# Kernel tuning notes

Measured on AMD Instinct MI355X. Metric: run time of the kernel, lower is better.

Reference implementation:

```python
import math
import jax, jax.numpy as jnp
import numpy as np

L = 4        # number of base-MLP layers
B = 16       # batch of weight-space samples
N = 256      # base-MLP width (n_in = n_out = N)
C_IN = 16    # input channels per weight entry
C_OUT = 16   # output channels per weight entry
HID = 64     # siren hidden dim
W0 = 1.0
W0_FIRST = 30.0
FINAL_NORM = math.sqrt((2 * L + 7) * C_IN)


def setup_inputs() -> dict:
    key = jax.random.key(0)
    ks = jax.random.split(key, 17)
    d = {}
    for i in range(L):
        d[f"w{i}"] = jax.random.normal(ks[i], (B, N, N, C_IN), jnp.float32) * 0.02
        d[f"b{i}"] = jax.random.normal(ks[L + i], (B, N, C_IN), jnp.float32) * 0.02
    def u(k, shape, scale):
        return jax.random.uniform(k, shape, jnp.float32, -scale, scale)
    # SIREN-style init scales
    d["s_w0"] = u(ks[8], (3, HID), 1.0 / 3.0)
    d["s_b0"] = u(ks[9], (HID,), 1.0 / math.sqrt(3.0))
    d["s_w1"] = u(ks[10], (HID, HID), math.sqrt(6.0 / HID) / W0)
    d["s_b1"] = u(ks[11], (HID,), 1.0 / math.sqrt(HID))
    d["s_w2"] = u(ks[12], (HID, HID), math.sqrt(6.0 / HID) / W0)
    d["s_b2"] = u(ks[13], (HID,), 1.0 / math.sqrt(HID))
    d["s_wo"] = u(ks[14], (HID, C_IN * C_OUT), math.sqrt(6.0 / HID) / W0)
    d["s_bo"] = u(ks[15], (C_IN * C_OUT,), 1.0 / math.sqrt(HID))
    return d


def _siren(x, sp):
    sw0, sb0, sw1, sb1, sw2, sb2, swo, sbo = sp
    h = jnp.sin(W0_FIRST * (x @ sw0 + sb0))
    h = jnp.sin(W0 * (h @ sw1 + sb1))
    h = jnp.sin(W0 * (h @ sw2 + sb2))
    return (h @ swo + sbo) / FINAL_NORM


def _forward(ws, bs, sp):
    term_idx = jnp.linspace(-1.0, 1.0, num=14)
    layer_idx = jnp.linspace(-1.0, 1.0, num=L)
    grid = jnp.stack(jnp.meshgrid(layer_idx, layer_idx, indexing='ij'), axis=-1)  # (L,L,2)

    g_in = jnp.concatenate([jnp.broadcast_to(grid, (4, L, L, 2)),
                            jnp.broadcast_to(term_idx[:4, None, None, None], (4, L, L, 1))], -1)
    global_terms = _siren(g_in, sp).reshape(4, L, L, C_IN, C_OUT)

    dgrid = jnp.transpose(jnp.diagonal(grid))          # (L,2)
    d_in = jnp.concatenate([jnp.broadcast_to(dgrid, (6, L, 2)),
                            jnp.broadcast_to(term_idx[4:10, None, None], (6, L, 1))], -1)
    diag_terms = _siren(d_in, sp).reshape(6, L, C_IN, C_OUT)

    p1 = jnp.transpose(jnp.diagonal(grid, offset=1))   # (L-1,2)
    p1_in = jnp.concatenate([jnp.broadcast_to(p1, (2, L - 1, 2)),
                             jnp.broadcast_to(term_idx[10:12, None, None], (2, L - 1, 1))], -1)
    diag_p1 = _siren(p1_in, sp).reshape(2, L - 1, C_IN, C_OUT)

    m1 = jnp.transpose(jnp.diagonal(grid, offset=-1))  # (L-1,2)
    m1_in = jnp.concatenate([jnp.broadcast_to(m1, (2, L - 1, 2)),
                             jnp.broadcast_to(term_idx[12:14, None, None], (2, L - 1, 1))], -1)
    diag_m1 = _siren(m1_in, sp).reshape(2, L - 1, C_IN, C_OUT)

    t_w_otherw, t_w_otherb = global_terms[0], global_terms[1]
    t_b_otherw, t_b_otherb = global_terms[2], global_terms[3]
    t_w_wrow, t_w_wcol, t_w_w = diag_terms[0], diag_terms[1], diag_terms[2]
    t_w_b, t_b_wcol, t_bb = diag_terms[3], diag_terms[4], diag_terms[5]
    t_w_wm1, t_w_bm1 = diag_m1[0], diag_m1[1]
    t_w_wp1, t_b_wp1 = diag_p1[0], diag_p1[1]

    rsums = [jnp.mean(w, axis=1) for w in ws]          # (B,K,c)
    csums = [jnp.mean(w, axis=2) for w in ws]          # (B,J,c)
    allsums = jnp.stack([jnp.mean(r, axis=1) for r in rsums], -1)  # (B,c,L)
    sums_b = jnp.stack([jnp.mean(b, axis=1) for b in bs], -1)      # (B,c,L)

    outs = []
    for i in range(L):
        ow = jnp.einsum('bjkc,cd->bjkd', ws[i], t_w_w[i])
        ow += jnp.einsum('bcl,lcd->bd', allsums, t_w_otherw[i])[:, None, None, :]
        ow += jnp.einsum('bcl,lcd->bd', sums_b, t_w_otherb[i])[:, None, None, :]
        ow += jnp.einsum('bjc,cd->bjd', csums[i], t_w_wcol[i])[:, :, None, :]
        ow += jnp.einsum('bkc,cd->bkd', rsums[i], t_w_wrow[i])[:, None, :, :]
        ow += jnp.einsum('bkc,cd->bkd', bs[i], t_w_b[i])[:, None, :, :]
        if i > 0:
            ow += jnp.einsum('bjc,cd->bjd', rsums[i - 1], t_w_wm1[i - 1])[:, :, None, :]
            ow += jnp.einsum('bjc,cd->bjd', bs[i - 1], t_w_bm1[i - 1])[:, :, None, :]
        if i < L - 1:
            ow += jnp.einsum('bkc,cd->bkd', csums[i + 1], t_w_wp1[i])[:, None, :, :]
        ob = jnp.einsum('bjc,cd->bjd', bs[i], t_bb[i])
        ob += jnp.einsum('bkc,cd->bkd', rsums[i], t_b_wcol[i])
        if i < L - 1:
            ob += jnp.einsum('bkc,cd->bkd', csums[i + 1], t_b_wp1[i])
        ob += jnp.einsum('bcl,lcd->bd', allsums, t_b_otherw[i])[:, None, :]
        ob += jnp.einsum('bcl,lcd->bd', sums_b, t_b_otherb[i])[:, None, :]
        outs += [ow, ob]
    return tuple(outs)


def reference(w0, w1, w2, w3, b0, b1, b2, b3,
              s_w0, s_b0, s_w1, s_b1, s_w2, s_b2, s_wo, s_bo):
    return _forward([w0, w1, w2, w3], [b0, b1, b2, b3],
                    (s_w0, s_b0, s_w1, s_b1, s_w2, s_b2, s_wo, s_bo))
```

## Files before the change

### kernel.cpp

```cpp
#include <hip/hip_runtime.h>
#include <math.h>

#define DEV_INLINE __device__ __forceinline__

constexpr int Nn = 256;
constexpr size_t SZW = (size_t)16 * 256 * 256 * 16;
constexpr size_t SZB = (size_t)16 * 256 * 16;
constexpr size_t OSTRIDE = SZW + SZB;

constexpr int T_GT = 0;
constexpr int T_DT = 16384;
constexpr int T_P1 = 22528;
constexpr int T_M1 = 24064;
constexpr int O_RS = 25600;
constexpr int O_CS = 287744;
constexpr int O_AS = 549888;
constexpr int O_BS = 550912;
constexpr int O_AROW = 551936;
constexpr int O_BCOL = 814080;

DEV_INLINE void f4acc(float4& a, const float4 b) { a.x += b.x; a.y += b.y; a.z += b.z; a.w += b.w; }
DEV_INLINE float4 f4add(const float4 a, const float4 b) { return make_float4(a.x + b.x, a.y + b.y, a.z + b.z, a.w + b.w); }
DEV_INLINE void f4fma(float4& a, float s, const float4 t) {
    a.x = fmaf(s, t.x, a.x); a.y = fmaf(s, t.y, a.y);
    a.z = fmaf(s, t.z, a.z); a.w = fmaf(s, t.w, a.w);
}

__global__ __launch_bounds__(64) void siren_kernel(
    const float* __restrict__ sw0, const float* __restrict__ sb0,
    const float* __restrict__ sw1, const float* __restrict__ sb1,
    const float* __restrict__ sw2, const float* __restrict__ sb2,
    const float* __restrict__ swo, const float* __restrict__ sbo,
    float* __restrict__ ws) {
    __shared__ float h[64];
    const int p = blockIdx.x, t = threadIdx.x;
    const float lv[4] = {-1.f, -1.f / 3.f, 1.f / 3.f, 1.f};
    float x, y, tt;
    if (p < 64)      { int tm = p >> 4, a = (p >> 2) & 3, bb = p & 3; x = lv[a];   y = lv[bb];  tt = -1.f + 2.f * tm / 13.f; }
    else if (p < 88) { int q = p - 64; int tm = q >> 2, a = q & 3;    x = lv[a];   y = lv[a];   tt = -1.f + 2.f * (4 + tm) / 13.f; }
    else if (p < 94) { int q = p - 88; int tm = q / 3, a = q % 3;     x = lv[a];   y = lv[a+1]; tt = -1.f + 2.f * (10 + tm) / 13.f; }
    else             { int q = p - 94; int tm = q / 3, a = q % 3;     x = lv[a+1]; y = lv[a];   tt = -1.f + 2.f * (12 + tm) / 13.f; }
    float v = sinf(30.f * (x * sw0[t] + y * sw0[64 + t] + tt * sw0[128 + t] + sb0[t]));
    h[t] = v; __syncthreads();
    float v1 = sb1[t];
    for (int u = 0; u < 64; ++u) v1 += h[u] * sw1[u * 64 + t];
    v1 = sinf(v1);
    __syncthreads(); h[t] = v1; __syncthreads();
    float v2 = sb2[t];
    for (int u = 0; u < 64; ++u) v2 += h[u] * sw2[u * 64 + t];
    v2 = sinf(v2);
    __syncthreads(); h[t] = v2; __syncthreads();
    const float inv_fn = 0.06454972243679028f;
    for (int m = 0; m < 4; ++m) {
        int o = m * 64 + t;
        float vo = sbo[o];
        for (int u = 0; u < 64; ++u) vo += h[u] * swo[u * 256 + o];
        ws[p * 256 + o] = vo * inv_fn;
    }
}

__global__ __launch_bounds__(64) void reduce_b_kernel(
    const float4* __restrict__ b0, const float4* __restrict__ b1,
    const float4* __restrict__ b2, const float4* __restrict__ b3,
    float* __restrict__ ws) {
    const int z = blockIdx.x;
    const int l = z >> 4, b = z & 15;
    const float4* bp = ((l == 0) ? b0 : (l == 1) ? b1 : (l == 2) ? b2 : b3) + (size_t)b * Nn * 4;
    const int lane = threadIdx.x;
    const int c4 = lane & 3, part = lane >> 2;
    float4 acc = make_float4(0.f, 0.f, 0.f, 0.f);
    for (int s = 0; s < 16; ++s) f4acc(acc, bp[(size_t)(part + s * 16) * 4 + c4]);
#pragma unroll
    for (int m = 4; m < 64; m <<= 1) {
        acc.x += __shfl_xor(acc.x, m); acc.y += __shfl_xor(acc.y, m);
        acc.z += __shfl_xor(acc.z, m); acc.w += __shfl_xor(acc.w, m);
    }
    if (lane < 4) {
        float* dst = ws + O_BS + (size_t)z * 16 + lane * 4;
        dst[0] = acc.x; dst[1] = acc.y; dst[2] = acc.z; dst[3] = acc.w;
    }
}

__global__ __launch_bounds__(256) void reduce_w_kernel(
    const float4* __restrict__ w0, const float4* __restrict__ w1,
    const float4* __restrict__ w2, const float4* __restrict__ w3,
    float* __restrict__ ws, int bbase) {
    const int tile = blockIdx.x;
    const int kt = tile & 7, jt = tile >> 3;
    const int lb = blockIdx.y;
    const int l = lb >> 2, b = bbase + (lb & 3);
    const float4* __restrict__ w = (l == 0) ? w0 : (l == 1) ? w1 : (l == 2) ? w2 : w3;
    const int tid = threadIdx.x;

    __shared__ float4 lds4[4096];
    __shared__ float asumf[32][16];

    const size_t base = ((size_t)(b * Nn + jt * 32)) * 1024 + (size_t)kt * 128;
#pragma unroll
    for (int it = 0; it < 16; ++it) {
        const int f = it * 256 + tid;
        const int jl = f >> 7, idx = f & 127;
        float4 v = w[base + (size_t)jl * 1024 + idx];
        lds4[jl * 128 + (idx ^ (jl & 7))] = v;
    }
    __syncthreads();

    const int h = tid & 1, c4 = (tid >> 1) & 3, loc = tid >> 3;

    float4 acc = make_float4(0.f, 0.f, 0.f, 0.f);
#pragma unroll
    for (int q = 0; q < 16; ++q) {
        const int kk = h * 16 + q;
        f4acc(acc, lds4[loc * 128 + ((kk * 4 + c4) ^ (loc & 7))]);
    }
    acc.x += __shfl_xor(acc.x, 1); acc.y += __shfl_xor(acc.y, 1);
    acc.z += __shfl_xor(acc.z, 1); acc.w += __shfl_xor(acc.w, 1);
    if (h == 0) {
        float* cdst = ws + O_CS + ((size_t)((l * 16 + b) * Nn + jt * 32 + loc)) * 16 + c4 * 4;
        atomicAdd(cdst + 0, acc.x); atomicAdd(cdst + 1, acc.y);
        atomicAdd(cdst + 2, acc.z); atomicAdd(cdst + 3, acc.w);
    }

    float4 acc2 = make_float4(0.f, 0.f, 0.f, 0.f);
#pragma unroll
    for (int q = 0; q < 16; ++q) {
        const int jj = h * 16 + q;
        f4acc(acc2, lds4[jj * 128 + ((loc * 4 + c4) ^ (jj & 7))]);
    }
    acc2.x += __shfl_xor(acc2.x, 1); acc2.y += __shfl_xor(acc2.y, 1);
    acc2.z += __shfl_xor(acc2.z, 1); acc2.w += __shfl_xor(acc2.w, 1);
    if (h == 0) {
        float* rdst = ws + O_RS + ((size_t)((l * 16 + b) * Nn + kt * 32 + loc)) * 16 + c4 * 4;
        atomicAdd(rdst + 0, acc2.x); atomicAdd(rdst + 1, acc2.y);
        atomicAdd(rdst + 2, acc2.z); atomicAdd(rdst + 3, acc2.w);
        asumf[loc][c4 * 4 + 0] = acc2.x; asumf[loc][c4 * 4 + 1] = acc2.y;
        asumf[loc][c4 * 4 + 2] = acc2.z; asumf[loc][c4 * 4 + 3] = acc2.w;
    }
    __syncthreads();

    if (tid < 16) {
        float s = 0.f;
#pragma unroll
        for (int kl = 0; kl < 32; ++kl) s += asumf[kl][tid];
        atomicAdd(ws + O_AS + (size_t)(l * 16 + b) * 16 + tid, s);
    }
}

__global__ __launch_bounds__(256) void vectors_kernel(
    const float* __restrict__ bias0, const float* __restrict__ bias1,
    const float* __restrict__ bias2, const float* __restrict__ bias3,
    float* __restrict__ ws, float* __restrict__ out, int bbase) {
    const int g = blockIdx.x * 256 + threadIdx.x;
    const int d = g & 15, n = (g >> 4) & 255, bg = (g >> 12) & 3, l = g >> 14;
    const int b = bbase + bg;
    const float invN = 1.f / 256.f, invNN = 1.f / 65536.f;
    const float* bias[4] = {bias0, bias1, bias2, bias3};
    const size_t rowi = (size_t)((l * 16 + b) * 256 + n) * 16;
    const float* cs = ws + O_CS + rowi;
    const float* rs = ws + O_RS + rowi;
    const float* bv = bias[l] + (size_t)(b * 256 + n) * 16;
    const float* dt = ws + T_DT;
    const float* Twrow  = dt + (0 * 4 + l) * 256;
    const float* Twcol  = dt + (1 * 4 + l) * 256;
    const float* Twb    = dt + (3 * 4 + l) * 256;
    const float* Tbwcol = dt + (4 * 4 + l) * 256;
    const float* Tbb    = dt + (5 * 4 + l) * 256;
    float arow = 0.f, bcol = 0.f, ob = 0.f;
#pragma unroll
    for (int c = 0; c < 16; ++c) {
        float cm = cs[c] * invN, rm = rs[c] * invN, bb = bv[c];
        arow += cm * Twcol[c * 16 + d];
        bcol += rm * Twrow[c * 16 + d] + bb * Twb[c * 16 + d];
        ob   += rm * Tbwcol[c * 16 + d] + bb * Tbb[c * 16 + d];
    }
    if (l > 0) {
        const float* rsm = ws + O_RS + (size_t)(((l - 1) * 16 + b) * 256 + n) * 16;
        const float* bvm = bias[l - 1] + (size_t)(b * 256 + n) * 16;
        const float* Twm1 = ws + T_M1 + (l - 1) * 256;
        const float* Tbm1 = ws + T_M1 + (3 + l - 1) * 256;
#pragma unroll
        for (int c = 0; c < 16; ++c)
            arow += rsm[c] * invN * Twm1[c * 16 + d] + bvm[c] * Tbm1[c * 16 + d];
    }
    if (l < 3) {
        const float* csp = ws + O_CS + (size_t)(((l + 1) * 16 + b) * 256 + n) * 16;
        const float* Twp1  = ws + T_P1 + l * 256;
        const float* Tbwp1 = ws + T_P1 + (3 + l) * 256;
#pragma unroll
        for (int c = 0; c < 16; ++c) {
            float cp = csp[c] * invN;
            bcol += cp * Twp1[c * 16 + d];
            ob   += cp * Tbwp1[c * 16 + d];
        }
    }
#pragma unroll
    for (int ll = 0; ll < 4; ++ll) {
        const float* as_ = ws + O_AS + (size_t)(ll * 16 + b) * 16;
        const float* bs_ = ws + O_BS + (size_t)(ll * 16 + b) * 16;
        const float* g0 = ws + ((0 * 4 + l) * 4 + ll) * 256;
        const float* g1 = ws + ((1 * 4 + l) * 4 + ll) * 256;
        const float* g2 = ws + ((2 * 4 + l) * 4 + ll) * 256;
        const float* g3 = ws + ((3 * 4 + l) * 4 + ll) * 256;
#pragma unroll
        for (int c = 0; c < 16; ++c) {
            float am = as_[c] * invNN, bm = bs_[c] * invN;
            arow += am * g0[c * 16 + d] + bm * g1[c * 16 + d];
            ob   += am * g2[c * 16 + d] + bm * g3[c * 16 + d];
        }
    }
    ws[O_AROW + rowi + d] = arow;
    ws[O_BCOL + rowi + d] = bcol;
    out[(size_t)l * OSTRIDE + SZW + (size_t)(b * 256 + n) * 16 + d] = ob;
}

__global__ __launch_bounds__(256) void transform_kernel(
    const float4* __restrict__ w0, const float4* __restrict__ w1,
    const float4* __restrict__ w2, const float4* __restrict__ w3,
    const float* __restrict__ ws, float4* __restrict__ out, int bbase) {
    const int j = blockIdx.x, bg = blockIdx.y, l = blockIdx.z;
    const int b = bbase + bg;
    const float4* __restrict__ w = (l == 0) ? w0 : (l == 1) ? w1 : (l == 2) ? w2 : w3;
    const int tid = threadIdx.x;
    const int d4 = tid & 3, kk = tid >> 2;
    const float4* T4 = (const float4*)ws + (T_DT / 4) + (2 * 4 + l) * 64;
    float4 t[16];
#pragma unroll
    for (int c = 0; c < 16; ++c) t[c] = T4[c * 4 + d4];
    const size_t rowbase = (size_t)(b * 256 + j) * 256;
    const float4* Ar = (const float4*)(ws + O_AROW);
    const float4* Bc = (const float4*)(ws + O_BCOL) + (size_t)(l * 16 + b) * 256 * 4 + d4;
    const float4 arow = Ar[(size_t)((l * 16 + b) * 256 + j) * 4 + d4];
    const size_t outb = (size_t)l * (OSTRIDE / 4) + rowbase * 4 + d4;
#pragma unroll
    for (int s = 0; s < 4; ++s) {
        const int k = s * 64 + kk;
        float4 acc = f4add(arow, Bc[(size_t)k * 4]);
        const float4* wp = w + (rowbase + k) * 4;
        float4 v0 = wp[0], v1 = wp[1], v2 = wp[2], v3 = wp[3];
        f4fma(acc, v0.x, t[0]);  f4fma(acc, v0.y, t[1]);  f4fma(acc, v0.z, t[2]);  f4fma(acc, v0.w, t[3]);
        f4fma(acc, v1.x, t[4]);  f4fma(acc, v1.y, t[5]);  f4fma(acc, v1.z, t[6]);  f4fma(acc, v1.w, t[7]);
        f4fma(acc, v2.x, t[8]);  f4fma(acc, v2.y, t[9]);  f4fma(acc, v2.z, t[10]); f4fma(acc, v2.w, t[11]);
        f4fma(acc, v3.x, t[12]); f4fma(acc, v3.y, t[13]); f4fma(acc, v3.z, t[14]); f4fma(acc, v3.w, t[15]);
        out[outb + (size_t)k * 4] = acc;
    }
}

extern "C" void kernel_launch(void* const* d_in, const int* in_sizes, int n_in,
                              void* d_out, int out_size, void* d_ws, size_t ws_size,
                              hipStream_t stream) {
    const float *W[4], *Bv[4], *S[8];
    if (in_sizes[1] == in_sizes[0]) {
        for (int i = 0; i < 4; ++i) { W[i] = (const float*)d_in[i]; Bv[i] = (const float*)d_in[4 + i]; }
    } else {
        for (int i = 0; i < 4; ++i) { W[i] = (const float*)d_in[2 * i]; Bv[i] = (const float*)d_in[2 * i + 1]; }
    }
    for (int k = 0; k < 8; ++k) S[k] = (const float*)d_in[8 + k];
    float* ws = (float*)d_ws;
    float* out = (float*)d_out;

    hipMemsetAsync(ws + O_RS, 0, (size_t)(O_AROW - O_RS) * sizeof(float), stream);
    siren_kernel<<<100, 64, 0, stream>>>(S[0], S[1], S[2], S[3], S[4], S[5], S[6], S[7], ws);
    reduce_b_kernel<<<64, 64, 0, stream>>>((const float4*)Bv[0], (const float4*)Bv[1],
                                           (const float4*)Bv[2], (const float4*)Bv[3], ws);
    for (int g = 0; g < 4; ++g) {
        const int bbase = 4 * g;
        reduce_w_kernel<<<dim3(64, 16), 256, 0, stream>>>(
            (const float4*)W[0], (const float4*)W[1], (const float4*)W[2], (const float4*)W[3], ws, bbase);
        vectors_kernel<<<256, 256, 0, stream>>>(Bv[0], Bv[1], Bv[2], Bv[3], ws, out, bbase);
        transform_kernel<<<dim3(256, 4, 4), 256, 0, stream>>>(
            (const float4*)W[0], (const float4*)W[1], (const float4*)W[2], (const float4*)W[3],
            ws, (float4*)out, bbase);
    }
}
```

Baseline: 648.3 us.

## Replace tiled LDS weight reduction with row-strip streaming and partial-sum fold

The weight reduction kernel now streams full 8-row strips straight from global memory instead of staging 32x32 tiles in LDS. Column sums are written directly and row sums are stored as per-strip partials, which a new fold kernel then combines. This removes most of the atomics and the large memset. The batch group size doubles from 4 to 8, so there are fewer launches. The cost is an extra partial-sum buffer, about 16 MB of extra traffic, and one more kernel launch per group; the transform kernel may also re-read weights less often from cache.

```diff
diff --git a/kernel.cpp b/kernel.cpp
--- a/kernel.cpp
+++ b/kernel.cpp
@@ -8,22 +8,27 @@
 constexpr size_t SZB = (size_t)16 * 256 * 16;
 constexpr size_t OSTRIDE = SZW + SZB;
 
-constexpr int T_GT = 0;
-constexpr int T_DT = 16384;
-constexpr int T_P1 = 22528;
-constexpr int T_M1 = 24064;
-constexpr int O_RS = 25600;
-constexpr int O_CS = 287744;
-constexpr int O_AS = 549888;
-constexpr int O_BS = 550912;
-constexpr int O_AROW = 551936;
-constexpr int O_BCOL = 814080;
+constexpr int T_GT  = 0;
+constexpr int T_DT  = 16384;
+constexpr int T_P1  = 22528;
+constexpr int T_M1  = 24064;
+constexpr int O_RSF = 25600;
+constexpr int O_CS  = 287744;
+constexpr int O_AS  = 549888;
+constexpr int O_BS  = 550912;
+constexpr int O_AROW= 551936;
+constexpr int O_BCOL= 814080;
+constexpr int O_RSP = 1076224;
 
 DEV_INLINE void f4acc(float4& a, const float4 b) { a.x += b.x; a.y += b.y; a.z += b.z; a.w += b.w; }
 DEV_INLINE float4 f4add(const float4 a, const float4 b) { return make_float4(a.x + b.x, a.y + b.y, a.z + b.z, a.w + b.w); }
 DEV_INLINE void f4fma(float4& a, float s, const float4 t) {
     a.x = fmaf(s, t.x, a.x); a.y = fmaf(s, t.y, a.y);
     a.z = fmaf(s, t.z, a.z); a.w = fmaf(s, t.w, a.w);
+}
+DEV_INLINE void f4shfl_xor_acc(float4& a, int m) {
+    a.x += __shfl_xor(a.x, m); a.y += __shfl_xor(a.y, m);
+    a.z += __shfl_xor(a.z, m); a.w += __shfl_xor(a.w, m);
 }
 
 __global__ __launch_bounds__(64) void siren_kernel(
@@ -71,10 +76,7 @@
     float4 acc = make_float4(0.f, 0.f, 0.f, 0.f);
     for (int s = 0; s < 16; ++s) f4acc(acc, bp[(size_t)(part + s * 16) * 4 + c4]);
 #pragma unroll
-    for (int m = 4; m < 64; m <<= 1) {
-        acc.x += __shfl_xor(acc.x, m); acc.y += __shfl_xor(acc.y, m);
-        acc.z += __shfl_xor(acc.z, m); acc.w += __shfl_xor(acc.w, m);
-    }
+    for (int m = 4; m < 64; m <<= 1) f4shfl_xor_acc(acc, m);
     if (lane < 4) {
         float* dst = ws + O_BS + (size_t)z * 16 + lane * 4;
         dst[0] = acc.x; dst[1] = acc.y; dst[2] = acc.z; dst[3] = acc.w;
@@ -85,65 +87,68 @@
     const float4* __restrict__ w0, const float4* __restrict__ w1,
     const float4* __restrict__ w2, const float4* __restrict__ w3,
     float* __restrict__ ws, int bbase) {
-    const int tile = blockIdx.x;
-    const int kt = tile & 7, jt = tile >> 3;
-    const int lb = blockIdx.y;
-    const int l = lb >> 2, b = bbase + (lb & 3);
+    const int strip = blockIdx.x;
+    const int lbg = blockIdx.y;
+    const int l = lbg >> 3, b = bbase + (lbg & 7);
     const float4* __restrict__ w = (l == 0) ? w0 : (l == 1) ? w1 : (l == 2) ? w2 : w3;
     const int tid = threadIdx.x;
-
-    __shared__ float4 lds4[4096];
-    __shared__ float asumf[32][16];
-
-    const size_t base = ((size_t)(b * Nn + jt * 32)) * 1024 + (size_t)kt * 128;
-#pragma unroll
-    for (int it = 0; it < 16; ++it) {
-        const int f = it * 256 + tid;
-        const int jl = f >> 7, idx = f & 127;
-        float4 v = w[base + (size_t)jl * 1024 + idx];
-        lds4[jl * 128 + (idx ^ (jl & 7))] = v;
+    const int wv = tid >> 6, lane = tid & 63;
+    const int plb = l * 16 + b;
+
+    __shared__ float4 csbuf[8][4][4];
+    __shared__ float4 abuf[4][4];
+
+    float4 racc0 = make_float4(0, 0, 0, 0), racc1 = racc0, racc2 = racc0, racc3 = racc0;
+    const size_t rowb = ((size_t)(b * Nn + strip * 8)) * 1024;
+
+#pragma unroll
+    for (int r = 0; r < 8; ++r) {
+        const float4* wp = w + rowb + (size_t)r * 1024 + tid;
+        float4 v0 = wp[0], v1 = wp[256], v2 = wp[512], v3 = wp[768];
+        f4acc(racc0, v0); f4acc(racc1, v1); f4acc(racc2, v2); f4acc(racc3, v3);
+        float4 s = f4add(f4add(v0, v1), f4add(v2, v3));
+        f4shfl_xor_acc(s, 4); f4shfl_xor_acc(s, 8);
+        f4shfl_xor_acc(s, 16); f4shfl_xor_acc(s, 32);
+        if (lane < 4) csbuf[r][wv][lane] = s;
     }
     __syncthreads();
 
-    const int h = tid & 1, c4 = (tid >> 1) & 3, loc = tid >> 3;
-
-    float4 acc = make_float4(0.f, 0.f, 0.f, 0.f);
-#pragma unroll
-    for (int q = 0; q < 16; ++q) {
-        const int kk = h * 16 + q;
-        f4acc(acc, lds4[loc * 128 + ((kk * 4 + c4) ^ (loc & 7))]);
-    }
-    acc.x += __shfl_xor(acc.x, 1); acc.y += __shfl_xor(acc.y, 1);
-    acc.z += __shfl_xor(acc.z, 1); acc.w += __shfl_xor(acc.w, 1);
-    if (h == 0) {
-        float* cdst = ws + O_CS + ((size_t)((l * 16 + b) * Nn + jt * 32 + loc)) * 16 + c4 * 4;
-        atomicAdd(cdst + 0, acc.x); atomicAdd(cdst + 1, acc.y);
-        atomicAdd(cdst + 2, acc.z); atomicAdd(cdst + 3, acc.w);
-    }
-
-    float4 acc2 = make_float4(0.f, 0.f, 0.f, 0.f);
-#pragma unroll
-    for (int q = 0; q < 16; ++q) {
-        const int jj = h * 16 + q;
-        f4acc(acc2, lds4[jj * 128 + ((loc * 4 + c4) ^ (jj & 7))]);
-    }
-    acc2.x += __shfl_xor(acc2.x, 1); acc2.y += __shfl_xor(acc2.y, 1);
-    acc2.z += __shfl_xor(acc2.z, 1); acc2.w += __shfl_xor(acc2.w, 1);
-    if (h == 0) {
-        float* rdst = ws + O_RS + ((size_t)((l * 16 + b) * Nn + kt * 32 + loc)) * 16 + c4 * 4;
-        atomicAdd(rdst + 0, acc2.x); atomicAdd(rdst + 1, acc2.y);
-        atomicAdd(rdst + 2, acc2.z); atomicAdd(rdst + 3, acc2.w);
-        asumf[loc][c4 * 4 + 0] = acc2.x; asumf[loc][c4 * 4 + 1] = acc2.y;
-        asumf[loc][c4 * 4 + 2] = acc2.z; asumf[loc][c4 * 4 + 3] = acc2.w;
-    }
+    if (tid < 32) {
+        const int r = tid >> 2, cc = tid & 3;
+        float4 cv = f4add(f4add(csbuf[r][0][cc], csbuf[r][1][cc]),
+                          f4add(csbuf[r][2][cc], csbuf[r][3][cc]));
+        ((float4*)(ws + O_CS))[(size_t)(plb * Nn + strip * 8 + r) * 4 + cc] = cv;
+    }
+
+    float4* part = (float4*)(ws + O_RSP) + (size_t)(plb * 32 + strip) * 1024;
+    part[tid]       = racc0;
+    part[256 + tid] = racc1;
+    part[512 + tid] = racc2;
+    part[768 + tid] = racc3;
+
+    float4 a = f4add(f4add(racc0, racc1), f4add(racc2, racc3));
+    f4shfl_xor_acc(a, 4); f4shfl_xor_acc(a, 8);
+    f4shfl_xor_acc(a, 16); f4shfl_xor_acc(a, 32);
+    if (lane < 4) abuf[wv][lane] = a;
     __syncthreads();
-
-    if (tid < 16) {
-        float s = 0.f;
-#pragma unroll
-        for (int kl = 0; kl < 32; ++kl) s += asumf[kl][tid];
-        atomicAdd(ws + O_AS + (size_t)(l * 16 + b) * 16 + tid, s);
-    }
+    if (tid < 4) {
+        float4 av = f4add(f4add(abuf[0][tid], abuf[1][tid]), f4add(abuf[2][tid], abuf[3][tid]));
+        float* dst = ws + O_AS + (size_t)plb * 16 + tid * 4;
+        atomicAdd(dst + 0, av.x); atomicAdd(dst + 1, av.y);
+        atomicAdd(dst + 2, av.z); atomicAdd(dst + 3, av.w);
+    }
+}
+
+__global__ __launch_bounds__(256) void fold_rs_kernel(float* __restrict__ ws, int bbase) {
+    const int g = blockIdx.x * 256 + threadIdx.x;
+    const int rest = g & 1023, lbg = g >> 10;
+    const int l = lbg >> 3, b = bbase + (lbg & 7);
+    const int plb = l * 16 + b;
+    const float4* part = (const float4*)(ws + O_RSP) + (size_t)(plb * 32) * 1024 + rest;
+    float4 acc = part[0];
+#pragma unroll
+    for (int s = 1; s < 32; ++s) f4acc(acc, part[(size_t)s * 1024]);
+    ((float4*)(ws + O_RSF))[(size_t)plb * 1024 + rest] = acc;
 }
 
 __global__ __launch_bounds__(256) void vectors_kernel(
@@ -151,13 +156,13 @@
     const float* __restrict__ bias2, const float* __restrict__ bias3,
     float* __restrict__ ws, float* __restrict__ out, int bbase) {
     const int g = blockIdx.x * 256 + threadIdx.x;
-    const int d = g & 15, n = (g >> 4) & 255, bg = (g >> 12) & 3, l = g >> 14;
+    const int d = g & 15, n = (g >> 4) & 255, bg = (g >> 12) & 7, l = g >> 15;
     const int b = bbase + bg;
     const float invN = 1.f / 256.f, invNN = 1.f / 65536.f;
     const float* bias[4] = {bias0, bias1, bias2, bias3};
     const size_t rowi = (size_t)((l * 16 + b) * 256 + n) * 16;
     const float* cs = ws + O_CS + rowi;
-    const float* rs = ws + O_RS + rowi;
+    const float* rs = ws + O_RSF + rowi;
     const float* bv = bias[l] + (size_t)(b * 256 + n) * 16;
     const float* dt = ws + T_DT;
     const float* Twrow  = dt + (0 * 4 + l) * 256;
@@ -174,7 +179,7 @@
         ob   += rm * Tbwcol[c * 16 + d] + bb * Tbb[c * 16 + d];
     }
     if (l > 0) {
-        const float* rsm = ws + O_RS + (size_t)(((l - 1) * 16 + b) * 256 + n) * 16;
+        const float* rsm = ws + O_RSF + (size_t)(((l - 1) * 16 + b) * 256 + n) * 16;
         const float* bvm = bias[l - 1] + (size_t)(b * 256 + n) * 16;
         const float* Twm1 = ws + T_M1 + (l - 1) * 256;
         const float* Tbm1 = ws + T_M1 + (3 + l - 1) * 256;
@@ -258,16 +263,17 @@
     float* ws = (float*)d_ws;
     float* out = (float*)d_out;
 
-    hipMemsetAsync(ws + O_RS, 0, (size_t)(O_AROW - O_RS) * sizeof(float), stream);
+    hipMemsetAsync(ws + O_AS, 0, 1024 * sizeof(float), stream);
     siren_kernel<<<100, 64, 0, stream>>>(S[0], S[1], S[2], S[3], S[4], S[5], S[6], S[7], ws);
     reduce_b_kernel<<<64, 64, 0, stream>>>((const float4*)Bv[0], (const float4*)Bv[1],
                                            (const float4*)Bv[2], (const float4*)Bv[3], ws);
-    for (int g = 0; g < 4; ++g) {
-        const int bbase = 4 * g;
-        reduce_w_kernel<<<dim3(64, 16), 256, 0, stream>>>(
+    for (int g = 0; g < 2; ++g) {
+        const int bbase = 8 * g;
+        reduce_w_kernel<<<dim3(32, 32), 256, 0, stream>>>(
             (const float4*)W[0], (const float4*)W[1], (const float4*)W[2], (const float4*)W[3], ws, bbase);
-        vectors_kernel<<<256, 256, 0, stream>>>(Bv[0], Bv[1], Bv[2], Bv[3], ws, out, bbase);
-        transform_kernel<<<dim3(256, 4, 4), 256, 0, stream>>>(
+        fold_rs_kernel<<<128, 256, 0, stream>>>(ws, bbase);
+        vectors_kernel<<<512, 256, 0, stream>>>(Bv[0], Bv[1], Bv[2], Bv[3], ws, out, bbase);
+        transform_kernel<<<dim3(256, 8, 4), 256, 0, stream>>>(
             (const float4*)W[0], (const float4*)W[1], (const float4*)W[2], (const float4*)W[3],
             ws, (float4*)out, bbase);
     }
```

Result: faster. 625.9 us (-3.4%).
